# Performance work log

Measured on AMD Instinct MI355X. Metric: run time of the kernel, lower is better.

## Reference

```python
import jax, jax.numpy as jnp
import numpy as np

N = 100_000   # nodes
E = 1_600_000 # edges (avg degree 16)
D = 128       # input_dim
H = 128       # hidden_dim
G = 64        # graphs in batch
C = 2         # num_classes


def setup_inputs() -> dict:
    key = jax.random.key(0)
    ks = jax.random.split(key, 16)
    x = jax.random.normal(ks[0], (N, D), dtype=jnp.float32)
    edge_index = jax.random.randint(ks[1], (2, E), 0, N, dtype=jnp.int32)
    batch = jnp.sort(jax.random.randint(ks[2], (N,), 0, G, dtype=jnp.int32))
    def lin(k, fin, fout):
        s = 1.0 / np.sqrt(fin)
        kw, kb = jax.random.split(k)
        W = jax.random.uniform(kw, (fin, fout), jnp.float32, -s, s)
        b = jax.random.uniform(kb, (fout,), jnp.float32, -s, s)
        return W, b
    W0, b0 = lin(ks[3], D, H)
    W1, b1 = lin(ks[4], H, H)
    W2, b2 = lin(ks[5], H, H)
    Wc1, bc1 = lin(ks[6], 2 * H, H)
    Wc2, bc2 = lin(ks[7], H, C)
    return dict(x=x, edge_index=edge_index, batch=batch,
                W0=W0, b0=b0, W1=W1, b1=b1, W2=W2, b2=b2,
                Wc1=Wc1, bc1=bc1, Wc2=Wc2, bc2=bc2)


def _gcn_layer(x, W, b, src, dst, dinv):
    # GCNConv with self-loops and symmetric normalization:
    # out_i = sum_{j->i} d_j^{-1/2} d_i^{-1/2} (x_j W) + d_i^{-1} (x_i W) + b
    h = x @ W                                   # [N, H]
    coef = dinv[src] * dinv[dst]                # [E]
    agg = jax.ops.segment_sum(h[src] * coef[:, None], dst, num_segments=N)
    return agg + h * (dinv * dinv)[:, None] + b


def reference(x, edge_index, batch, W0, b0, W1, b1, W2, b2, Wc1, bc1, Wc2, bc2):
    src, dst = edge_index[0], edge_index[1]
    # degree with self-loops (in-degree on target nodes + 1)
    deg = jax.ops.segment_sum(jnp.ones((E,), jnp.float32), dst, num_segments=N) + 1.0
    dinv = jax.lax.rsqrt(deg)
    for W, b in ((W0, b0), (W1, b1), (W2, b2)):
        x = jax.nn.relu(_gcn_layer(x, W, b, src, dst, dinv))
        # dropout: inference mode -> identity
    # global mean pool per graph
    sums = jax.ops.segment_sum(x, batch, num_segments=G)            # [G, H]
    cnt = jax.ops.segment_sum(jnp.ones((N,), jnp.float32), batch, num_segments=G)
    pooled = sums / jnp.maximum(cnt, 1.0)[:, None]
    combined = jnp.concatenate([pooled, pooled], axis=1)            # [G, 2H]
    hcls = jax.nn.relu(combined @ Wc1 + bc1)
    return hcls @ Wc2 + bc2                                         # [G, C]
```

## Files before the change

### kernel.cpp

```cpp
#include <hip/hip_runtime.h>

#define HDIM 128
#define GCOUNT 64
#define CHUNK 2048

__device__ __forceinline__ float bfl(unsigned u) { return __uint_as_float(u << 16); }
__device__ __forceinline__ float bfh(unsigned u) { return __uint_as_float(u & 0xffff0000u); }
__device__ __forceinline__ unsigned short f2bf(float f) {
  unsigned u = __float_as_uint(f);
  unsigned r = (u + 0x7fffu + ((u >> 16) & 1u)) >> 16;
  return (unsigned short)r;
}
__device__ __forceinline__ unsigned pk2(float a, float b) {
  return (unsigned)f2bf(a) | ((unsigned)f2bf(b) << 16);
}

typedef __attribute__((ext_vector_type(8))) short short8;
typedef __attribute__((ext_vector_type(4))) float f32x4;

__device__ __forceinline__ unsigned qb(float v, float rinv) {
  int q = (int)rintf(v * rinv);
  return (unsigned)(q & 0xff);
}


__global__ void mega1(const float* __restrict__ W0, const float* __restrict__ W1,
                      const float* __restrict__ W2,
                      unsigned short* __restrict__ h0, unsigned short* __restrict__ l0,
                      unsigned short* __restrict__ h1, unsigned short* __restrict__ l1,
                      unsigned short* __restrict__ h2, unsigned short* __restrict__ l2,
                      float* __restrict__ pooled, float* __restrict__ gcnt, int pz,
                      const int* __restrict__ dst, int E, int G, int NB1,
                      int* __restrict__ gcount,
                      const float* __restrict__ x, uint2* __restrict__ S,
                      float* __restrict__ cs_base, int n) {
  __shared__ int hist[512];
  int b = blockIdx.x, t = threadIdx.x;
  if (b < 192) {
    int w = b >> 6;
    int idx = (b & 63) * 256 + t;
    const float* W = (w == 0) ? W0 : (w == 1) ? W1 : W2;
    unsigned short* hi = (w == 0) ? h0 : (w == 1) ? h1 : h2;
    unsigned short* lo = (w == 0) ? l0 : (w == 1) ? l1 : l2;
    int k = idx >> 7, nn = idx & 127;
    float wv = W[idx];
    unsigned short h = f2bf(wv);
    float hf = __uint_as_float((unsigned)h << 16);
    unsigned short l = f2bf(wv - hf);
    hi[nn * 128 + k] = h;
    lo[nn * 128 + k] = l;
  } else if (b < 192 + pz) {
    int i = (b - 192) * 256 + t;
    if (i < GCOUNT * HDIM) pooled[i] = 0.f;
    else if (i - GCOUNT * HDIM < GCOUNT) gcnt[i - GCOUNT * HDIM] = 0.f;
  } else if (b < 192 + pz + G) {
    int blk = b - 192 - pz;
    for (int i = t; i < NB1; i += 256) hist[i] = 0;
    __syncthreads();
    int base = blk * CHUNK;
    #pragma unroll
    for (int j = 0; j < CHUNK / 256; j++) {
      int e = base + j * 256 + t;
      if (e < E) atomicAdd(&hist[dst[e] >> 8], 1);
    }
    __syncthreads();
    for (int i = t; i < NB1; i += 256) gcount[i * G + blk] = hist[i];
  } else {
    int idx = (b - 192 - pz - G) * 16 + (t >> 4);
    int l = t & 15;
    int ridx = min(idx, n - 1);
    float4 f0 = ((const float4*)x)[(size_t)ridx * 32 + l * 2];
    float4 f1 = ((const float4*)x)[(size_t)ridx * 32 + l * 2 + 1];
    float v0 = f0.x, v1 = f0.y, v2 = f0.z, v3 = f0.w;
    float v4 = f1.x, v5 = f1.y, v6 = f1.z, v7 = f1.w;
    float mx = fmaxf(fmaxf(fmaxf(fabsf(v0), fabsf(v1)), fmaxf(fabsf(v2), fabsf(v3))),
                     fmaxf(fmaxf(fabsf(v4), fabsf(v5)), fmaxf(fabsf(v6), fabsf(v7))));
    mx = fmaxf(mx, __shfl_xor(mx, 1));
    mx = fmaxf(mx, __shfl_xor(mx, 2));
    mx = fmaxf(mx, __shfl_xor(mx, 4));
    mx = fmaxf(mx, __shfl_xor(mx, 8));
    float c = mx * (1.0f / 127.0f);
    float rinv = (mx > 0.f) ? 127.0f / mx : 0.f;
    if (idx < n) {
      unsigned lo = qb(v0, rinv) | (qb(v1, rinv) << 8) | (qb(v2, rinv) << 16) | (qb(v3, rinv) << 24);
      unsigned hi = qb(v4, rinv) | (qb(v5, rinv) << 8) | (qb(v6, rinv) << 16) | (qb(v7, rinv) << 24);
      S[(size_t)idx * 16 + l] = make_uint2(lo, hi);
      if (l == 0) cs_base[idx] = c;
    }
  }
}


__global__ void scanA(int* __restrict__ g, int* __restrict__ bsum, int M) {
  __shared__ int sh[1024];
  int t = threadIdx.x;
  int i = blockIdx.x * 1024 + t;
  int v = (i < M) ? g[i] : 0;
  sh[t] = v;
  __syncthreads();
  for (int off = 1; off < 1024; off <<= 1) {
    int u = (t >= off) ? sh[t - off] : 0;
    __syncthreads();
    sh[t] += u;
    __syncthreads();
  }
  if (i < M) g[i] = sh[t] - v;
  if (t == 1023) bsum[blockIdx.x] = sh[1023];
}

__global__ void scanB(int* __restrict__ g, const int* __restrict__ bsum, int nb, int M) {
  __shared__ int sh[512];
  int t = threadIdx.x;
  if (t < 512) sh[t] = (t < nb) ? bsum[t] : 0;
  __syncthreads();
  for (int off = 1; off < 512; off <<= 1) {
    int u = (t < 512 && t >= off) ? sh[t - off] : 0;
    __syncthreads();
    if (t < 512) sh[t] += u;
    __syncthreads();
  }
  #pragma unroll
  for (int k = 0; k < 2; k++) {
    int i = blockIdx.x * 2048 + k * 1024 + t;
    if (i < M) {
      int j = i >> 10;
      if (j) g[i] += sh[j - 1];
    }
  }
}


__global__ void rs_scatter(const int* __restrict__ src, const int* __restrict__ dst,
                           const int* __restrict__ gscan, int E, int G, int NB1,
                           uint2* __restrict__ sp) {
  __shared__ int run[512];
  int blk = blockIdx.x, t = threadIdx.x;
  for (int i = t; i < NB1; i += 256) run[i] = gscan[i * G + blk];
  __syncthreads();
  int base = blk * CHUNK;
  #pragma unroll
  for (int j = 0; j < CHUNK / 256; j++) {
    int e = base + j * 256 + t;
    if (e < E) {
      int d = dst[e];
      int pos = atomicAdd(&run[d >> 8], 1);
      sp[pos] = make_uint2((unsigned)d, (unsigned)src[e]);
    }
  }
}


__global__ void csr_fine(const uint2* __restrict__ sp, const int* __restrict__ gscan,
                         int E, int G, int NB1,
                         int* __restrict__ rowp, int* __restrict__ colv,
                         float* __restrict__ dinv, const float* __restrict__ cs_base,
                         float* __restrict__ cs, int n) {
  __shared__ int hist[256];
  __shared__ int scn[256];
  __shared__ int run2[256];
  int hb = blockIdx.x, t = threadIdx.x;
  int O = gscan[hb * G];
  int Oe = (hb == NB1 - 1) ? E : gscan[(hb + 1) * G];
  if (t < 256) hist[t] = 0;
  __syncthreads();
  for (int e = O + t; e < Oe; e += 512) atomicAdd(&hist[sp[e].x & 255], 1);
  __syncthreads();
  int v = 0;
  if (t < 256) { v = hist[t]; scn[t] = v; }
  __syncthreads();
  for (int off = 1; off < 256; off <<= 1) {
    int u = (t < 256 && t >= off) ? scn[t - off] : 0;
    __syncthreads();
    if (t < 256) scn[t] += u;
    __syncthreads();
  }
  if (t < 256) {
    int excl = scn[t] - v;
    run2[t] = O + excl;
    int d = (hb << 8) + t;
    rowp[d] = O + excl;
    if (d < n) {
      float dv = rsqrtf((float)v + 1.0f);
      dinv[d] = dv;
      cs[d] = cs_base[d] * dv;
    }
  }
  if (hb == NB1 - 1 && t == 0) rowp[n] = E;
  __syncthreads();
  for (int e = O + t; e < Oe; e += 512) {
    uint2 p = sp[e];
    int pos = atomicAdd(&run2[p.x & 255], 1);
    colv[pos] = (int)p.y;
  }
}


__device__ __forceinline__ void acc8(uint2 v, float c, float* a) {
  int xx = (int)v.x, yy = (int)v.y;
  a[0] += c * (float)(signed char)(xx);
  a[1] += c * (float)(signed char)(xx >> 8);
  a[2] += c * (float)(signed char)(xx >> 16);
  a[3] += c * (float)(xx >> 24);
  a[4] += c * (float)(signed char)(yy);
  a[5] += c * (float)(signed char)(yy >> 8);
  a[6] += c * (float)(signed char)(yy >> 16);
  a[7] += c * (float)(yy >> 24);
}

__global__ void agg_i8(const uint2* __restrict__ S, const float* __restrict__ cs,
                       const float* __restrict__ dinv,
                       const int* __restrict__ rowp, const int* __restrict__ col,
                       uint4* __restrict__ OUT, int n) {
  int g = (blockIdx.x * blockDim.x + threadIdx.x) >> 4;
  int lane = threadIdx.x & 15;
  if (g >= n) return;
  float a[8];
  {
    uint2 q = S[(size_t)g * 16 + lane];
    float c = cs[g];
    int xx = (int)q.x, yy = (int)q.y;
    a[0] = c * (float)(signed char)(xx);
    a[1] = c * (float)(signed char)(xx >> 8);
    a[2] = c * (float)(signed char)(xx >> 16);
    a[3] = c * (float)(xx >> 24);
    a[4] = c * (float)(signed char)(yy);
    a[5] = c * (float)(signed char)(yy >> 8);
    a[6] = c * (float)(signed char)(yy >> 16);
    a[7] = c * (float)(yy >> 24);
  }
  int e0 = rowp[g], e1 = rowp[g + 1];
  int e = e0;
  for (; e + 7 < e1; e += 8) {
    int s0 = col[e],     s1 = col[e + 1], s2 = col[e + 2], s3 = col[e + 3];
    int s4 = col[e + 4], s5 = col[e + 5], s6 = col[e + 6], s7 = col[e + 7];
    uint2 q0 = S[(size_t)s0 * 16 + lane];
    uint2 q1 = S[(size_t)s1 * 16 + lane];
    uint2 q2 = S[(size_t)s2 * 16 + lane];
    uint2 q3 = S[(size_t)s3 * 16 + lane];
    uint2 q4 = S[(size_t)s4 * 16 + lane];
    uint2 q5 = S[(size_t)s5 * 16 + lane];
    uint2 q6 = S[(size_t)s6 * 16 + lane];
    uint2 q7 = S[(size_t)s7 * 16 + lane];
    float c0 = cs[s0], c1 = cs[s1], c2 = cs[s2], c3 = cs[s3];
    float c4 = cs[s4], c5 = cs[s5], c6 = cs[s6], c7 = cs[s7];
    acc8(q0, c0, a); acc8(q1, c1, a); acc8(q2, c2, a); acc8(q3, c3, a);
    acc8(q4, c4, a); acc8(q5, c5, a); acc8(q6, c6, a); acc8(q7, c7, a);
  }
  for (; e + 3 < e1; e += 4) {
    int s0 = col[e], s1 = col[e + 1], s2 = col[e + 2], s3 = col[e + 3];
    uint2 q0 = S[(size_t)s0 * 16 + lane];
    uint2 q1 = S[(size_t)s1 * 16 + lane];
    uint2 q2 = S[(size_t)s2 * 16 + lane];
    uint2 q3 = S[(size_t)s3 * 16 + lane];
    float c0 = cs[s0], c1 = cs[s1], c2 = cs[s2], c3 = cs[s3];
    acc8(q0, c0, a); acc8(q1, c1, a); acc8(q2, c2, a); acc8(q3, c3, a);
  }
  for (; e < e1; e++) {
    int s = col[e];
    uint2 q = S[(size_t)s * 16 + lane];
    acc8(q, cs[s], a);
  }
  float d = dinv[g];
  uint4 o;
  o.x = pk2(a[0] * d, a[1] * d); o.y = pk2(a[2] * d, a[3] * d);
  o.z = pk2(a[4] * d, a[5] * d); o.w = pk2(a[6] * d, a[7] * d);
  OUT[(size_t)g * 16 + lane] = o;
}


__global__ __launch_bounds__(256) void gemm_mfma_q8(
    const uint4* __restrict__ A, const uint4* __restrict__ WThi, const uint4* __restrict__ WTlo,
    const float* __restrict__ bias, const float* __restrict__ dinv,
    unsigned char* __restrict__ Sout, float* __restrict__ csout, int n) {
  __shared__ char smem[34816];
  __shared__ float Lc[64];
  uint4* Wl = (uint4*)smem;
  int t = threadIdx.x;
  int lane = t & 63, wv = t >> 6;
  int m = lane & 15, quad = lane >> 4;
  int block0 = blockIdx.x * 64;
  int arow = block0 + wv * 16 + m;
  uint4 av[4];
  #pragma unroll
  for (int kb = 0; kb < 4; kb++)
    av[kb] = (arow < n) ? A[(size_t)arow * 16 + kb * 4 + quad] : make_uint4(0, 0, 0, 0);
  f32x4 acc[8];
  #pragma unroll
  for (int i = 0; i < 8; i++) acc[i] = (f32x4){0.f, 0.f, 0.f, 0.f};

  #pragma unroll
  for (int i = 0; i < 8; i++) {
    int idx = t + i * 256;
    Wl[(idx >> 4) * 17 + (idx & 15)] = WThi[idx];
  }
  __syncthreads();
  #pragma unroll
  for (int kb = 0; kb < 4; kb++) {
    short8 af = __builtin_bit_cast(short8, av[kb]);
    #pragma unroll
    for (int nt = 0; nt < 8; nt++) {
      uint4 bh = Wl[(nt * 16 + m) * 17 + kb * 4 + quad];
      acc[nt] = __builtin_amdgcn_mfma_f32_16x16x32_bf16(af, __builtin_bit_cast(short8, bh), acc[nt], 0, 0, 0);
    }
  }
  __syncthreads();
  #pragma unroll
  for (int i = 0; i < 8; i++) {
    int idx = t + i * 256;
    Wl[(idx >> 4) * 17 + (idx & 15)] = WTlo[idx];
  }
  __syncthreads();
  #pragma unroll
  for (int kb = 0; kb < 4; kb++) {
    short8 af = __builtin_bit_cast(short8, av[kb]);
    #pragma unroll
    for (int nt = 0; nt < 8; nt++) {
      uint4 bl = Wl[(nt * 16 + m) * 17 + kb * 4 + quad];
      acc[nt] = __builtin_amdgcn_mfma_f32_16x16x32_bf16(af, __builtin_bit_cast(short8, bl), acc[nt], 0, 0, 0);
    }
  }
  __syncthreads();

  #pragma unroll
  for (int r = 0; r < 4; r++) {
    int lrow = wv * 16 + quad * 4 + r;
    int grow = block0 + lrow;
    float sc = (grow < n) ? dinv[grow] : 0.f;
    float v[8];
    float mx = 0.f;
    #pragma unroll
    for (int nt = 0; nt < 8; nt++) {
      v[nt] = fmaxf(acc[nt][r] + bias[nt * 16 + m], 0.f) * sc;
      mx = fmaxf(mx, v[nt]);
    }
    mx = fmaxf(mx, __shfl_xor(mx, 1));
    mx = fmaxf(mx, __shfl_xor(mx, 2));
    mx = fmaxf(mx, __shfl_xor(mx, 4));
    mx = fmaxf(mx, __shfl_xor(mx, 8));
    float c = mx * (1.0f / 127.0f);
    float rinv = (mx > 0.f) ? 127.0f / mx : 0.f;
    #pragma unroll
    for (int nt = 0; nt < 8; nt++) {
      smem[lrow * 144 + nt * 16 + m] = (char)(int)rintf(v[nt] * rinv);
    }
    if (m == 0) Lc[lrow] = c;
  }
  __syncthreads();
  for (int i = t; i < 512; i += 256) {
    int lrow = i >> 3, seg = i & 7;
    int grow = block0 + lrow;
    if (grow < n)
      ((uint4*)Sout)[(size_t)grow * 8 + seg] = *(const uint4*)&smem[lrow * 144 + seg * 16];
  }
  if (t < 64 && block0 + t < n) csout[block0 + t] = Lc[t];
}


__global__ __launch_bounds__(256) void gemm_mfma(
    const uint4* __restrict__ A, const uint4* __restrict__ WThi, const uint4* __restrict__ WTlo,
    const float* __restrict__ bias, unsigned short* __restrict__ Y, int n) {
  __shared__ char smem[34816];
  uint4* Wl = (uint4*)smem;
  int t = threadIdx.x;
  int lane = t & 63, wv = t >> 6;
  int m = lane & 15, quad = lane >> 4;
  int block0 = blockIdx.x * 64;
  int arow = block0 + wv * 16 + m;
  uint4 av[4];
  #pragma unroll
  for (int kb = 0; kb < 4; kb++)
    av[kb] = (arow < n) ? A[(size_t)arow * 16 + kb * 4 + quad] : make_uint4(0, 0, 0, 0);
  f32x4 acc[8];
  #pragma unroll
  for (int i = 0; i < 8; i++) acc[i] = (f32x4){0.f, 0.f, 0.f, 0.f};

  #pragma unroll
  for (int i = 0; i < 8; i++) {
    int idx = t + i * 256;
    Wl[(idx >> 4) * 17 + (idx & 15)] = WThi[idx];
  }
  __syncthreads();
  #pragma unroll
  for (int kb = 0; kb < 4; kb++) {
    short8 af = __builtin_bit_cast(short8, av[kb]);
    #pragma unroll
    for (int nt = 0; nt < 8; nt++) {
      uint4 bh = Wl[(nt * 16 + m) * 17 + kb * 4 + quad];
      acc[nt] = __builtin_amdgcn_mfma_f32_16x16x32_bf16(af, __builtin_bit_cast(short8, bh), acc[nt], 0, 0, 0);
    }
  }
  __syncthreads();
  #pragma unroll
  for (int i = 0; i < 8; i++) {
    int idx = t + i * 256;
    Wl[(idx >> 4) * 17 + (idx & 15)] = WTlo[idx];
  }
  __syncthreads();
  #pragma unroll
  for (int kb = 0; kb < 4; kb++) {
    short8 af = __builtin_bit_cast(short8, av[kb]);
    #pragma unroll
    for (int nt = 0; nt < 8; nt++) {
      uint4 bl = Wl[(nt * 16 + m) * 17 + kb * 4 + quad];
      acc[nt] = __builtin_amdgcn_mfma_f32_16x16x32_bf16(af, __builtin_bit_cast(short8, bl), acc[nt], 0, 0, 0);
    }
  }
  __syncthreads();

  unsigned short* Ls = (unsigned short*)smem;
  #pragma unroll
  for (int r = 0; r < 4; r++) {
    int lrow = wv * 16 + quad * 4 + r;
    #pragma unroll
    for (int nt = 0; nt < 8; nt++) {
      float v = fmaxf(acc[nt][r] + bias[nt * 16 + m], 0.f);
      Ls[lrow * 136 + nt * 16 + m] = f2bf(v);
    }
  }
  __syncthreads();
  for (int i = t; i < 1024; i += 256) {
    int lrow = i >> 4, seg = i & 15;
    int grow = block0 + lrow;
    if (grow < n)
      ((uint4*)Y)[(size_t)grow * 16 + seg] = *(const uint4*)&smem[lrow * 272 + seg * 16];
  }
}


__global__ void pool_kernel(const unsigned short* __restrict__ X, const int* __restrict__ batch,
                            float* __restrict__ pooled, float* __restrict__ gcnt, int n) {
  int t = threadIdx.x;
  int r0 = blockIdx.x * 64;
  if (r0 >= n) return;
  int r1 = min(r0 + 64, n);
  int g = batch[r0];
  float acc = 0.f, cl = 0.f;
  for (int r = r0; r < r1; r++) {
    int gr = batch[r];
    if (gr != g) {
      atomicAdd(&pooled[g * HDIM + t], acc);
      if (t == 0) atomicAdd(&gcnt[g], cl);
      acc = 0.f; cl = 0.f; g = gr;
    }
    acc += __uint_as_float((unsigned)X[(size_t)r * HDIM + t] << 16);
    cl += 1.f;
  }
  atomicAdd(&pooled[g * HDIM + t], acc);
  if (t == 0) atomicAdd(&gcnt[g], cl);
}


__global__ void cls_kernel(const float* __restrict__ pooled, const float* __restrict__ gcnt,
                           const float* __restrict__ Wc1, const float* __restrict__ bc1,
                           const float* __restrict__ Wc2, const float* __restrict__ bc2,
                           float* __restrict__ out) {
  __shared__ float p[HDIM];
  __shared__ float r0s[HDIM], r1s[HDIM];
  int g = blockIdx.x, t = threadIdx.x;
  float c = fmaxf(gcnt[g], 1.0f);
  p[t] = pooled[g * HDIM + t] / c;
  __syncthreads();
  float acc = bc1[t];
  for (int k = 0; k < HDIM; k++) {
    acc += p[k] * (Wc1[k * HDIM + t] + Wc1[(HDIM + k) * HDIM + t]);
  }
  float h = fmaxf(acc, 0.f);
  r0s[t] = h * Wc2[t * 2 + 0];
  r1s[t] = h * Wc2[t * 2 + 1];
  __syncthreads();
  for (int s2 = 64; s2 > 0; s2 >>= 1) {
    if (t < s2) { r0s[t] += r0s[t + s2]; r1s[t] += r1s[t + s2]; }
    __syncthreads();
  }
  if (t == 0) {
    out[g * 2 + 0] = r0s[0] + bc2[0];
    out[g * 2 + 1] = r1s[0] + bc2[1];
  }
}


extern "C" void kernel_launch(void* const* d_in, const int* in_sizes, int n_in,
                              void* d_out, int out_size, void* d_ws, size_t ws_size,
                              hipStream_t stream) {
  const float* x   = (const float*)d_in[0];
  const int*   ei  = (const int*)d_in[1];
  const int*   bat = (const int*)d_in[2];
  const float* W0  = (const float*)d_in[3];
  const float* b0  = (const float*)d_in[4];
  const float* W1  = (const float*)d_in[5];
  const float* b1  = (const float*)d_in[6];
  const float* W2  = (const float*)d_in[7];
  const float* b2  = (const float*)d_in[8];
  const float* Wc1 = (const float*)d_in[9];
  const float* bc1 = (const float*)d_in[10];
  const float* Wc2 = (const float*)d_in[11];
  const float* bc2 = (const float*)d_in[12];
  float* out = (float*)d_out;

  int N = in_sizes[0] / HDIM;
  int E = in_sizes[1] / 2;
  const int* src = ei;
  const int* dst = ei + E;

  int NB1 = (N + 255) >> 8;
  int G = (E + CHUNK - 1) / CHUNK;
  int M = NB1 * G;

  char* ws = (char*)d_ws;
  size_t off = 0;
  auto alloc = [&](size_t bytes) -> void* {
    void* p = (void*)(ws + off);
    off += (bytes + 511) & ~(size_t)511;
    return p;
  };
  unsigned char* Sa = (unsigned char*)alloc((size_t)N * HDIM * 2);
  unsigned char* Sb = Sa + (size_t)N * HDIM;
  unsigned short* H = (unsigned short*)Sa;
  unsigned short* Abuf = (unsigned short*)alloc((size_t)N * HDIM * 2);
  float* csa  = (float*)alloc((size_t)N * 4);
  float* csb  = (float*)alloc((size_t)N * 4);
  float* cs_base = (float*)alloc((size_t)N * 4);
  float* dinv = (float*)alloc((size_t)N * 4);
  int*   rowp = (int*)alloc((size_t)(NB1 * 256 + 2) * 4);
  int*   colv = (int*)alloc((size_t)E * 4);
  uint2* sp   = (uint2*)alloc((size_t)E * 8);
  float* pooled = (float*)alloc((size_t)GCOUNT * HDIM * 4);
  float* gcnt   = (float*)alloc((size_t)GCOUNT * 4);
  unsigned short* wt_hi[3], *wt_lo[3];
  for (int i = 0; i < 3; i++) {
    wt_hi[i] = (unsigned short*)alloc(HDIM * HDIM * 2);
    wt_lo[i] = (unsigned short*)alloc(HDIM * HDIM * 2);
  }
  int* gcount = (int*)alloc((size_t)(M + 2) * 4);
  int nbM = (M + 1023) / 1024;
  int* bsum = (int*)alloc((size_t)nbM * 4);

  int pz = (GCOUNT * HDIM + GCOUNT + 255) / 256;
  int psb = (N + 15) / 16;
  mega1<<<192 + pz + G + psb, 256, 0, stream>>>(W0, W1, W2,
      wt_hi[0], wt_lo[0], wt_hi[1], wt_lo[1], wt_hi[2], wt_lo[2],
      pooled, gcnt, pz, dst, E, G, NB1, gcount,
      x, (uint2*)Sa, cs_base, N);

  scanA<<<nbM, 1024, 0, stream>>>(gcount, bsum, M);
  scanB<<<(M + 2047) / 2048, 1024, 0, stream>>>(gcount, bsum, nbM, M);

  rs_scatter<<<G, 256, 0, stream>>>(src, dst, gcount, E, G, NB1, sp);
  csr_fine<<<NB1, 512, 0, stream>>>(sp, gcount, E, G, NB1, rowp, colv,
      dinv, cs_base, csa, N);

  int aggBlocks = (N + 15) / 16;
  int gemmBlocks = (N + 63) / 64;

  agg_i8<<<aggBlocks, 256, 0, stream>>>((const uint2*)Sa, csa, dinv, rowp, colv, (uint4*)Abuf, N);
  gemm_mfma_q8<<<gemmBlocks, 256, 0, stream>>>((const uint4*)Abuf, (const uint4*)wt_hi[0],
      (const uint4*)wt_lo[0], b0, dinv, Sb, csb, N);

  agg_i8<<<aggBlocks, 256, 0, stream>>>((const uint2*)Sb, csb, dinv, rowp, colv, (uint4*)Abuf, N);
  gemm_mfma_q8<<<gemmBlocks, 256, 0, stream>>>((const uint4*)Abuf, (const uint4*)wt_hi[1],
      (const uint4*)wt_lo[1], b1, dinv, Sa, csa, N);

  agg_i8<<<aggBlocks, 256, 0, stream>>>((const uint2*)Sa, csa, dinv, rowp, colv, (uint4*)Abuf, N);
  gemm_mfma<<<gemmBlocks, 256, 0, stream>>>((const uint4*)Abuf, (const uint4*)wt_hi[2],
      (const uint4*)wt_lo[2], b2, H, N);

  pool_kernel<<<(N + 63) / 64, 128, 0, stream>>>(H, bat, pooled, gcnt, N);
  cls_kernel<<<GCOUNT, HDIM, 0, stream>>>(pooled, gcnt, Wc1, bc1, Wc2, bc2, out);
}
```

Baseline: 362.6 us.

## Switch to offset-binary uint8 features and fold scanB into consumers

New measurement: 367.3 us. No clear change (+1.3%).

```diff
diff --git a/kernel.cpp b/kernel.cpp
--- a/kernel.cpp
+++ b/kernel.cpp
@@ -18,8 +18,8 @@
 typedef __attribute__((ext_vector_type(8))) short short8;
 typedef __attribute__((ext_vector_type(4))) float f32x4;
 
-__device__ __forceinline__ unsigned qb(float v, float rinv) {
-  int q = (int)rintf(v * rinv);
+__device__ __forceinline__ unsigned qbu(float v, float rinv) {
+  int q = (int)rintf(v * rinv) + 128;
   return (unsigned)(q & 0xff);
 }
 
@@ -82,8 +82,8 @@
     float c = mx * (1.0f / 127.0f);
     float rinv = (mx > 0.f) ? 127.0f / mx : 0.f;
     if (idx < n) {
-      unsigned lo = qb(v0, rinv) | (qb(v1, rinv) << 8) | (qb(v2, rinv) << 16) | (qb(v3, rinv) << 24);
-      unsigned hi = qb(v4, rinv) | (qb(v5, rinv) << 8) | (qb(v6, rinv) << 16) | (qb(v7, rinv) << 24);
+      unsigned lo = qbu(v0, rinv) | (qbu(v1, rinv) << 8) | (qbu(v2, rinv) << 16) | (qbu(v3, rinv) << 24);
+      unsigned hi = qbu(v4, rinv) | (qbu(v5, rinv) << 8) | (qbu(v6, rinv) << 16) | (qbu(v7, rinv) << 24);
       S[(size_t)idx * 16 + l] = make_uint2(lo, hi);
       if (l == 0) cs_base[idx] = c;
     }
@@ -108,39 +108,32 @@
   if (t == 1023) bsum[blockIdx.x] = sh[1023];
 }
 
-__global__ void scanB(int* __restrict__ g, const int* __restrict__ bsum, int nb, int M) {
-  __shared__ int sh[512];
-  int t = threadIdx.x;
-  if (t < 512) sh[t] = (t < nb) ? bsum[t] : 0;
-  __syncthreads();
-  for (int off = 1; off < 512; off <<= 1) {
-    int u = (t < 512 && t >= off) ? sh[t - off] : 0;
-    __syncthreads();
-    if (t < 512) sh[t] += u;
-    __syncthreads();
-  }
-  #pragma unroll
-  for (int k = 0; k < 2; k++) {
-    int i = blockIdx.x * 2048 + k * 1024 + t;
-    if (i < M) {
-      int j = i >> 10;
-      if (j) g[i] += sh[j - 1];
-    }
-  }
-}
-
 
 __global__ void rs_scatter(const int* __restrict__ src, const int* __restrict__ dst,
-                           const int* __restrict__ gscan, int E, int G, int NB1,
-                           uint2* __restrict__ sp) {
+                           const int* __restrict__ gA, const int* __restrict__ bsum,
+                           int nbM, int E, int G, int NB1, uint2* __restrict__ sp) {
+  __shared__ int bs[512];
   __shared__ int run[512];
   int blk = blockIdx.x, t = threadIdx.x;
-  for (int i = t; i < NB1; i += 256) run[i] = gscan[i * G + blk];
+  int v = (t < nbM) ? bsum[t] : 0;
+  bs[t] = v;
+  __syncthreads();
+  for (int off = 1; off < 512; off <<= 1) {
+    int u = (t >= off) ? bs[t - off] : 0;
+    __syncthreads();
+    bs[t] += u;
+    __syncthreads();
+  }
+  for (int i = t; i < NB1; i += 512) {
+    int idx = i * G + blk;
+    int j = idx >> 10;
+    run[i] = gA[idx] + (j ? bs[j - 1] : 0);
+  }
   __syncthreads();
   int base = blk * CHUNK;
   #pragma unroll
-  for (int j = 0; j < CHUNK / 256; j++) {
-    int e = base + j * 256 + t;
+  for (int j = 0; j < CHUNK / 512; j++) {
+    int e = base + j * 512 + t;
     if (e < E) {
       int d = dst[e];
       int pos = atomicAdd(&run[d >> 8], 1);
@@ -150,17 +143,36 @@
 }
 
 
-__global__ void csr_fine(const uint2* __restrict__ sp, const int* __restrict__ gscan,
+__global__ void csr_fine(const uint2* __restrict__ sp, const int* __restrict__ gA,
+                         const int* __restrict__ bsum, int nbM,
                          int E, int G, int NB1,
                          int* __restrict__ rowp, int* __restrict__ colv,
                          float* __restrict__ dinv, const float* __restrict__ cs_base,
                          float* __restrict__ cs, int n) {
+  __shared__ int bs[512];
   __shared__ int hist[256];
   __shared__ int scn[256];
   __shared__ int run2[256];
   int hb = blockIdx.x, t = threadIdx.x;
-  int O = gscan[hb * G];
-  int Oe = (hb == NB1 - 1) ? E : gscan[(hb + 1) * G];
+  int v0 = (t < nbM) ? bsum[t] : 0;
+  bs[t] = v0;
+  __syncthreads();
+  for (int off = 1; off < 512; off <<= 1) {
+    int u = (t >= off) ? bs[t - off] : 0;
+    __syncthreads();
+    bs[t] += u;
+    __syncthreads();
+  }
+  int idx0 = hb * G;
+  int j0 = idx0 >> 10;
+  int O = gA[idx0] + (j0 ? bs[j0 - 1] : 0);
+  int Oe;
+  if (hb == NB1 - 1) Oe = E;
+  else {
+    int idx1 = (hb + 1) * G;
+    int j1 = idx1 >> 10;
+    Oe = gA[idx1] + (j1 ? bs[j1 - 1] : 0);
+  }
   if (t < 256) hist[t] = 0;
   __syncthreads();
   for (int e = O + t; e < Oe; e += 512) atomicAdd(&hist[sp[e].x & 255], 1);
@@ -195,16 +207,16 @@
 }
 
 
-__device__ __forceinline__ void acc8(uint2 v, float c, float* a) {
-  int xx = (int)v.x, yy = (int)v.y;
-  a[0] += c * (float)(signed char)(xx);
-  a[1] += c * (float)(signed char)(xx >> 8);
-  a[2] += c * (float)(signed char)(xx >> 16);
-  a[3] += c * (float)(xx >> 24);
-  a[4] += c * (float)(signed char)(yy);
-  a[5] += c * (float)(signed char)(yy >> 8);
-  a[6] += c * (float)(signed char)(yy >> 16);
-  a[7] += c * (float)(yy >> 24);
+__device__ __forceinline__ void accu8(uint2 v, float c, float* a) {
+  unsigned x = v.x, y = v.y;
+  a[0] += c * (float)(x & 0xffu);
+  a[1] += c * (float)((x >> 8) & 0xffu);
+  a[2] += c * (float)((x >> 16) & 0xffu);
+  a[3] += c * (float)(x >> 24);
+  a[4] += c * (float)(y & 0xffu);
+  a[5] += c * (float)((y >> 8) & 0xffu);
+  a[6] += c * (float)((y >> 16) & 0xffu);
+  a[7] += c * (float)(y >> 24);
 }
 
 __global__ void agg_i8(const uint2* __restrict__ S, const float* __restrict__ cs,
@@ -214,38 +226,16 @@
   int g = (blockIdx.x * blockDim.x + threadIdx.x) >> 4;
   int lane = threadIdx.x & 15;
   if (g >= n) return;
-  float a[8];
+  float a[8] = {0.f, 0.f, 0.f, 0.f, 0.f, 0.f, 0.f, 0.f};
+  float csum;
   {
     uint2 q = S[(size_t)g * 16 + lane];
     float c = cs[g];
-    int xx = (int)q.x, yy = (int)q.y;
-    a[0] = c * (float)(signed char)(xx);
-    a[1] = c * (float)(signed char)(xx >> 8);
-    a[2] = c * (float)(signed char)(xx >> 16);
-    a[3] = c * (float)(xx >> 24);
-    a[4] = c * (float)(signed char)(yy);
-    a[5] = c * (float)(signed char)(yy >> 8);
-    a[6] = c * (float)(signed char)(yy >> 16);
-    a[7] = c * (float)(yy >> 24);
+    csum = c;
+    accu8(q, c, a);
   }
   int e0 = rowp[g], e1 = rowp[g + 1];
   int e = e0;
-  for (; e + 7 < e1; e += 8) {
-    int s0 = col[e],     s1 = col[e + 1], s2 = col[e + 2], s3 = col[e + 3];
-    int s4 = col[e + 4], s5 = col[e + 5], s6 = col[e + 6], s7 = col[e + 7];
-    uint2 q0 = S[(size_t)s0 * 16 + lane];
-    uint2 q1 = S[(size_t)s1 * 16 + lane];
-    uint2 q2 = S[(size_t)s2 * 16 + lane];
-    uint2 q3 = S[(size_t)s3 * 16 + lane];
-    uint2 q4 = S[(size_t)s4 * 16 + lane];
-    uint2 q5 = S[(size_t)s5 * 16 + lane];
-    uint2 q6 = S[(size_t)s6 * 16 + lane];
-    uint2 q7 = S[(size_t)s7 * 16 + lane];
-    float c0 = cs[s0], c1 = cs[s1], c2 = cs[s2], c3 = cs[s3];
-    float c4 = cs[s4], c5 = cs[s5], c6 = cs[s6], c7 = cs[s7];
-    acc8(q0, c0, a); acc8(q1, c1, a); acc8(q2, c2, a); acc8(q3, c3, a);
-    acc8(q4, c4, a); acc8(q5, c5, a); acc8(q6, c6, a); acc8(q7, c7, a);
-  }
   for (; e + 3 < e1; e += 4) {
     int s0 = col[e], s1 = col[e + 1], s2 = col[e + 2], s3 = col[e + 3];
     uint2 q0 = S[(size_t)s0 * 16 + lane];
@@ -253,17 +243,23 @@
     uint2 q2 = S[(size_t)s2 * 16 + lane];
     uint2 q3 = S[(size_t)s3 * 16 + lane];
     float c0 = cs[s0], c1 = cs[s1], c2 = cs[s2], c3 = cs[s3];
-    acc8(q0, c0, a); acc8(q1, c1, a); acc8(q2, c2, a); acc8(q3, c3, a);
+    accu8(q0, c0, a); accu8(q1, c1, a); accu8(q2, c2, a); accu8(q3, c3, a);
+    csum += c0 + c1 + c2 + c3;
   }
   for (; e < e1; e++) {
     int s = col[e];
     uint2 q = S[(size_t)s * 16 + lane];
-    acc8(q, cs[s], a);
+    float c = cs[s];
+    accu8(q, c, a);
+    csum += c;
   }
   float d = dinv[g];
+  float boff = 128.f * csum;
   uint4 o;
-  o.x = pk2(a[0] * d, a[1] * d); o.y = pk2(a[2] * d, a[3] * d);
-  o.z = pk2(a[4] * d, a[5] * d); o.w = pk2(a[6] * d, a[7] * d);
+  o.x = pk2((a[0] - boff) * d, (a[1] - boff) * d);
+  o.y = pk2((a[2] - boff) * d, (a[3] - boff) * d);
+  o.z = pk2((a[4] - boff) * d, (a[5] - boff) * d);
+  o.w = pk2((a[6] - boff) * d, (a[7] - boff) * d);
   OUT[(size_t)g * 16 + lane] = o;
 }
 
@@ -341,7 +337,7 @@
     float rinv = (mx > 0.f) ? 127.0f / mx : 0.f;
     #pragma unroll
     for (int nt = 0; nt < 8; nt++) {
-      smem[lrow * 144 + nt * 16 + m] = (char)(int)rintf(v[nt] * rinv);
+      smem[lrow * 144 + nt * 16 + m] = (char)(unsigned char)(((int)rintf(v[nt] * rinv) + 128) & 0xff);
     }
     if (m == 0) Lc[lrow] = c;
   }
@@ -533,7 +529,7 @@
   }
   int* gcount = (int*)alloc((size_t)(M + 2) * 4);
   int nbM = (M + 1023) / 1024;
-  int* bsum = (int*)alloc((size_t)nbM * 4);
+  int* bsum = (int*)alloc((size_t)(nbM + 2) * 4);
 
   int pz = (GCOUNT * HDIM + GCOUNT + 255) / 256;
   int psb = (N + 15) / 16;
@@ -543,10 +539,9 @@
       x, (uint2*)Sa, cs_base, N);
 
   scanA<<<nbM, 1024, 0, stream>>>(gcount, bsum, M);
-  scanB<<<(M + 2047) / 2048, 1024, 0, stream>>>(gcount, bsum, nbM, M);
-
-  rs_scatter<<<G, 256, 0, stream>>>(src, dst, gcount, E, G, NB1, sp);
-  csr_fine<<<NB1, 512, 0, stream>>>(sp, gcount, E, G, NB1, rowp, colv,
+
+  rs_scatter<<<G, 512, 0, stream>>>(src, dst, gcount, bsum, nbM, E, G, NB1, sp);
+  csr_fine<<<NB1, 512, 0, stream>>>(sp, gcount, bsum, nbM, E, G, NB1, rowp, colv,
       dinv, cs_base, csa, N);
 
   int aggBlocks = (N + 15) / 16;
```
